# Optimization experiments

Hardware: AMD Instinct MI355X
Metric: run time of the kernel (lower is better)

The kernel has to match this reference:

```python
import jax, jax.numpy as jnp
import numpy as np

VOCAB, EMBED, HID, SEQ, BATCH = 32000, 256, 512, 128, 256
U1, U2 = 256, 64


def setup_inputs() -> dict:
    key = jax.random.key(0)
    ks = jax.random.split(key, 8)
    s = 0.05  # small init scale keeps relu-LSTM states bounded
    return {
        "inputs": jax.random.randint(ks[0], (BATCH, SEQ), 0, VOCAB),
        "emb": jax.random.normal(ks[1], (VOCAB, EMBED), jnp.float32) * s,
        "W": jax.random.normal(ks[2], (EMBED, 4 * HID), jnp.float32) * s,
        "U": jax.random.normal(ks[3], (HID, 4 * HID), jnp.float32) * s,
        "b": jnp.zeros((4 * HID,), jnp.float32),
        "W2": jax.random.normal(ks[4], (HID, U1), jnp.float32) * s,
        "b2": jnp.zeros((U1,), jnp.float32),
        "W3": jax.random.normal(ks[5], (U1, U2), jnp.float32) * s,
        "b3": jnp.zeros((U2,), jnp.float32),
    }


def reference(inputs, emb, W, U, b, W2, b2, W3, b3):
    H = U.shape[0]
    x = emb[inputs]                      # [B, T, E] embedding lookup
    xW = jnp.einsum('bte,eg->btg', x, W) + b  # precompute input gate projections [B, T, 4H]

    def step(carry, xw_t):
        h, c = carry
        z = xw_t + h @ U                 # [B, 4H]; Keras gate order i, f, c, o
        i = jax.nn.sigmoid(z[:, :H])
        f = jax.nn.sigmoid(z[:, H:2 * H])
        g = jax.nn.relu(z[:, 2 * H:3 * H])   # activation='relu'
        o = jax.nn.sigmoid(z[:, 3 * H:])
        c = f * c + i * g
        h = o * jax.nn.relu(c)
        return (h, c), None

    B = x.shape[0]
    init = (jnp.zeros((B, H), x.dtype), jnp.zeros((B, H), x.dtype))
    (h, _), _ = jax.lax.scan(step, init, jnp.swapaxes(xW, 0, 1))  # scan over time

    y = jax.nn.relu(h @ W2 + b2)         # Dense head 1
    return jax.nn.softmax(y @ W3 + b3, axis=-1)  # Dense head 2 (softmax)
```

## Files before the change

kernel.cpp:

```cpp
#include <hip/hip_runtime.h>
#include <hip/hip_bf16.h>
#include <stdint.h>

#define B_  256
#define T_  128
#define E_  256
#define H_  512
#define G4  2048
#define U1_ 256
#define U2_ 64

#define HB_STEP   (16 * 16 * 64 * 8)
#define XF_STEP   (16 * 8 * 64 * 8)
#define SGN 0x8000800080008000ULL

typedef __attribute__((ext_vector_type(8))) short bf16x8;
typedef __attribute__((ext_vector_type(4))) float f32x4;
typedef __attribute__((ext_vector_type(2))) unsigned long long ullx2;
typedef unsigned long long ull;

static __device__ __forceinline__ unsigned short f2bf(float f) {
    unsigned u = __float_as_uint(f);
    unsigned r = (u + 0x7FFFu + ((u >> 16) & 1u)) >> 16;
    return (unsigned short)r;
}
static __device__ __forceinline__ ull ald(const ull* p) {
    return __hip_atomic_load(p, __ATOMIC_RELAXED, __HIP_MEMORY_SCOPE_AGENT);
}
static __device__ __forceinline__ void ast(ull* p, ull v) {
    __hip_atomic_store(p, v, __ATOMIC_RELAXED, __HIP_MEMORY_SCOPE_AGENT);
}

__global__ __launch_bounds__(256) void k_prep(const float* __restrict__ U,
                                              const float* __restrict__ W,
                                              short* __restrict__ wpk) {
    __shared__ float ld[32][64];
    const int bj = blockIdx.x;
    const int g  = bj >> 3;
    const int l0 = (bj & 7) * 64;
    const int t  = threadIdx.x;
    const int p   = t >> 4;
    const int hsl = p >> 1, blk = p & 1;
    const int ci  = t & 3;
    const int g4w = (t >> 2) & 3;
    const int hs  = (l0 >> 3) + hsl;
    const int c16 = g * 4 + ci;
    const int jloc = hsl * 8 + blk * 4 + ci;
    for (int kc = 0; kc < 24; ++kc) {
        const float* src = (kc < 16) ? (U + (long)(kc * 32) * G4)
                                     : (W + (long)((kc - 16) * 32) * G4);
        #pragma unroll
        for (int r = 0; r < 8; ++r) {
            int row = r * 4 + (t >> 6);
            ld[row][t & 63] = src[(long)row * G4 + g * 512 + l0 + (t & 63)];
        }
        __syncthreads();
        bf16x8 o;
        #pragma unroll
        for (int e = 0; e < 8; ++e) o[e] = (short)f2bf(ld[g4w * 8 + e][jloc]);
        *(bf16x8*)(wpk + (((long)(hs * 2 + blk) * 24 + kc) * 64 + (g4w * 16 + c16)) * 8) = o;
        __syncthreads();
    }
}

__global__ __launch_bounds__(256) void k_gather(const int* __restrict__ inp,
                                                const float* __restrict__ emb,
                                                short* __restrict__ xfrag) {
    const int tid  = threadIdx.x;
    const int wv   = tid >> 6;
    const int lane = tid & 63;
    const int c16  = lane & 15;
    const int g4   = lane >> 4;
    for (int it = 0; it < 16; ++it) {
        int task  = (it * 256 + blockIdx.x) * 4 + wv;
        int kc    = task & 7;
        int btile = (task >> 3) & 15;
        int t     = task >> 7;
        int b     = btile * 16 + c16;
        int idx   = inp[b * T_ + t];
        const float* src = emb + (long)idx * E_ + kc * 32 + g4 * 8;
        float4 v0 = *(const float4*)src;
        float4 v1 = *(const float4*)(src + 4);
        bf16x8 o;
        o[0]=(short)f2bf(v0.x); o[1]=(short)f2bf(v0.y); o[2]=(short)f2bf(v0.z); o[3]=(short)f2bf(v0.w);
        o[4]=(short)f2bf(v1.x); o[5]=(short)f2bf(v1.y); o[6]=(short)f2bf(v1.z); o[7]=(short)f2bf(v1.w);
        *(bf16x8*)(xfrag + ((long)((t * 16 + btile) * 8 + kc) * 64 + lane) * 8) = o;
    }
}

__global__ __launch_bounds__(256, 1) void k_lstm(
    const float* __restrict__ bias,
    const short* __restrict__ wpk,
    const short* __restrict__ xfrag,
    short* hfrag,
    float* hfin)
{
    __shared__ short lds[2][16][64][8];
    const int tid  = threadIdx.x;
    const int wid  = blockIdx.x;
    const int bt   = wid >> 4;
    const int hsg  = wid & 15;
    const int lane = tid & 63;
    const int wv   = tid >> 6;
    const int hs   = hsg * 4 + wv;
    const int c16  = lane & 15;
    const int g4   = lane >> 4;
    const int selfj = ((hsg >> 2) == wv) ? (hsg & 3) : -1;

    bf16x8 a_u[2][16], a_w[2][8];
    #pragma unroll
    for (int blk = 0; blk < 2; ++blk) {
        #pragma unroll
        for (int kc = 0; kc < 16; ++kc)
            a_u[blk][kc] = *(const bf16x8*)(wpk + (((long)(hs*2+blk)*24 + kc)*64 + lane)*8);
        #pragma unroll
        for (int kc = 0; kc < 8; ++kc)
            a_w[blk][kc] = *(const bf16x8*)(wpk + (((long)(hs*2+blk)*24 + 16 + kc)*64 + lane)*8);
    }
    float b0[4], b1[4];
    #pragma unroll
    for (int q = 0; q < 4; ++q) {
        b0[q] = bias[g4 * H_ + hs * 8 + q];
        b1[q] = bias[g4 * H_ + hs * 8 + 4 + q];
    }
    float cst[8];
    #pragma unroll
    for (int i = 0; i < 8; ++i) cst[i] = 0.f;

    ull* const pub0 = (ull*)hfrag + (((long)bt * 16 + hsg) * 64 + wv * 16 + c16) * 2;

    for (int t = 0; t < T_; ++t) {
        const int cb = t & 1;
        ull L[4] = {0,0,0,0}, Hh[4] = {0,0,0,0};
        const ull* hp = (const ull*)hfrag + ((long)(t - 1) * HB_STEP) / 4;
        if (t > 0) {
            #pragma unroll
            for (int j = 0; j < 4; ++j) {
                const ull* p = hp + (((long)bt * 16 + (wv * 4 + j)) * 64 + lane) * 2;
                L[j]  = ald(p);
                Hh[j] = ald(p + 1);
            }
        }

        const short* xr = xfrag + (long)t * XF_STEP;
        bf16x8 xf[8];
        #pragma unroll
        for (int kc = 0; kc < 8; ++kc)
            xf[kc] = *(const bf16x8*)(xr + ((long)(bt * 8 + kc) * 64 + lane) * 8);

        f32x4 a0 = (f32x4){b0[0], b0[1], b0[2], b0[3]};
        f32x4 a1 = (f32x4){b1[0], b1[1], b1[2], b1[3]};
        #pragma unroll
        for (int kc = 0; kc < 8; ++kc) {
            a0 = __builtin_amdgcn_mfma_f32_16x16x32_bf16(a_w[0][kc], xf[kc], a0, 0, 0, 0);
            a1 = __builtin_amdgcn_mfma_f32_16x16x32_bf16(a_w[1][kc], xf[kc], a1, 0, 0, 0);
        }

        if (t > 0) {
            unsigned stale = 0xFu & ~((selfj >= 0) ? (1u << selfj) : 0u);
            for (int guard = 0; guard < (1 << 20); ++guard) {
                unsigned ns = 0;
                #pragma unroll
                for (int j = 0; j < 4; ++j) {
                    if ((stale >> j) & 1u) {
                        if (!__all(((L[j] | Hh[j]) & SGN) == 0)) ns |= (1u << j);
                    }
                }
                stale = ns;
                if (!stale) break;
                #pragma unroll
                for (int j = 0; j < 4; ++j) {
                    if ((stale >> j) & 1u) {
                        const ull* p = hp + (((long)bt * 16 + (wv * 4 + j)) * 64 + lane) * 2;
                        L[j]  = ald(p);
                        Hh[j] = ald(p + 1);
                    }
                }
            }
            #pragma unroll
            for (int j = 0; j < 4; ++j) {
                if (j != selfj) {
                    ullx2 u; u[0] = L[j]; u[1] = Hh[j];
                    *(ullx2*)(&lds[cb][wv * 4 + j][lane][0]) = u;
                }
            }
        }
        __syncthreads();

        if (t > 0) {
            #pragma unroll
            for (int kc = 0; kc < 16; ++kc) {
                bf16x8 hf = *(const bf16x8*)(&lds[cb][kc][lane][0]);
                a0 = __builtin_amdgcn_mfma_f32_16x16x32_bf16(a_u[0][kc], hf, a0, 0, 0, 0);
                a1 = __builtin_amdgcn_mfma_f32_16x16x32_bf16(a_u[1][kc], hf, a1, 0, 0, 0);
            }
        }

        float hv[8];
        #pragma unroll
        for (int blk = 0; blk < 2; ++blk) {
            #pragma unroll
            for (int q = 0; q < 4; ++q) {
                float z = blk ? a1[q] : a0[q];
                float a = (g4 == 2) ? fmaxf(z, 0.f)
                                    : 1.f / (1.f + __expf(-z));
                float ai = __shfl(a, c16,      64);
                float af = __shfl(a, c16 + 16, 64);
                float ag = __shfl(a, c16 + 32, 64);
                float ao = __shfl(a, c16 + 48, 64);
                float c_ = af * cst[blk*4+q] + ai * ag;
                cst[blk*4+q] = c_;
                hv[blk*4+q] = ao * fmaxf(c_, 0.f);
            }
        }

        if (t < T_ - 1) {
            if (g4 == 0) {
                ull p0 = (ull)f2bf(hv[0]) | ((ull)f2bf(hv[1])<<16)
                       | ((ull)f2bf(hv[2])<<32) | ((ull)f2bf(hv[3])<<48);
                ull p1 = (ull)f2bf(hv[4]) | ((ull)f2bf(hv[5])<<16)
                       | ((ull)f2bf(hv[6])<<32) | ((ull)f2bf(hv[7])<<48);
                ull* d = pub0 + (long)t * (HB_STEP / 4);
                ast(d, p0); ast(d + 1, p1);
                ullx2 u; u[0] = p0; u[1] = p1;
                *(ullx2*)(&lds[(t + 1) & 1][hsg][wv * 16 + c16][0]) = u;
            }
        } else {
            if (g4 == 0) {
                *(float4*)(hfin + ((long)bt * 16 + c16) * H_ + hs * 8)
                    = make_float4(hv[0], hv[1], hv[2], hv[3]);
                *(float4*)(hfin + ((long)bt * 16 + c16) * H_ + hs * 8 + 4)
                    = make_float4(hv[4], hv[5], hv[6], hv[7]);
            }
        }
    }
}

__global__ __launch_bounds__(256) void k_head(const float* __restrict__ hfin,
                                              const float* __restrict__ W2,
                                              const float* __restrict__ b2,
                                              const float* __restrict__ W3,
                                              const float* __restrict__ b3,
                                              float* __restrict__ out) {
    __shared__ float hs[H_];
    __shared__ float ys[U1_];
    __shared__ float ps[4][U2_];
    const int b = blockIdx.x, tid = threadIdx.x;
    if (tid < 128) *(float4*)(hs + tid * 4) = *(const float4*)(hfin + (long)b * H_ + tid * 4);
    __syncthreads();
    float acc = b2[tid];
    #pragma unroll 8
    for (int k = 0; k < H_; ++k) acc += hs[k] * W2[(long)k * U1_ + tid];
    ys[tid] = fmaxf(acc, 0.f);
    __syncthreads();
    const int u2 = tid & 63, part = tid >> 6;
    float p = 0.f;
    #pragma unroll 8
    for (int k = part * 64; k < part * 64 + 64; ++k) p += ys[k] * W3[(long)k * U2_ + u2];
    ps[part][u2] = p;
    __syncthreads();
    if (tid < 64) {
        float lg = b3[tid] + ps[0][tid] + ps[1][tid] + ps[2][tid] + ps[3][tid];
        float m = lg;
        #pragma unroll
        for (int off = 32; off >= 1; off >>= 1) m = fmaxf(m, __shfl_xor(m, off, 64));
        float e = __expf(lg - m);
        float s = e;
        #pragma unroll
        for (int off = 32; off >= 1; off >>= 1) s += __shfl_xor(s, off, 64);
        out[(long)b * U2_ + tid] = e / s;
    }
}

extern "C" void kernel_launch(void* const* d_in, const int* in_sizes, int n_in,
                              void* d_out, int out_size, void* d_ws, size_t ws_size,
                              hipStream_t stream) {
    const int*   inp = (const int*)d_in[0];
    const float* emb = (const float*)d_in[1];
    const float* W   = (const float*)d_in[2];
    const float* U   = (const float*)d_in[3];
    const float* bb  = (const float*)d_in[4];
    const float* W2  = (const float*)d_in[5];
    const float* b2  = (const float*)d_in[6];
    const float* W3  = (const float*)d_in[7];
    const float* b3  = (const float*)d_in[8];

    char* ws = (char*)d_ws;
    const long HB_BYTES = (long)(T_ - 1) * HB_STEP * 2;
    short* hfrag = (short*)ws;
    short* xfrag = (short*)(ws + HB_BYTES);
    short* wpk   = (short*)(ws + HB_BYTES + 16777216);
    float* hfin  = (float*)(ws + HB_BYTES + 16777216 + 3145728);

    hipMemsetAsync(hfrag, 0xAA, HB_BYTES, stream);
    k_prep<<<32, 256, 0, stream>>>(U, W, wpk);
    k_gather<<<256, 256, 0, stream>>>(inp, emb, xfrag);
    k_lstm<<<256, 256, 0, stream>>>(bb, wpk, xfrag, hfrag, hfin);
    k_head<<<B_, 256, 0, stream>>>(hfin, W2, b2, W3, b3, (float*)d_out);
}
```

Measured before the change: 528.6 us.

## Use 512-thread LSTM blocks covering 64 hidden units each, halving grid size

The persistent LSTM kernel now runs 128 blocks of 8 waves instead of 256 blocks of 4 waves. Each block owns two K-chunks of the hidden state, so each wave polls only two remote h fragments per step, and the wave whose chunks are local skips polling. The goal is less cross-block flag polling and global traffic per step, since more of the recurrent state is exchanged through LDS. In exchange, fewer CUs are used and the 8-wave __syncthreads barrier is wider, and each wave still keeps its full register-resident weight slices.

```diff
diff --git a/kernel.cpp b/kernel.cpp
--- a/kernel.cpp
+++ b/kernel.cpp
@@ -88,7 +88,7 @@
     }
 }
 
-__global__ __launch_bounds__(256, 1) void k_lstm(
+__global__ __launch_bounds__(512, 1) void k_lstm(
     const float* __restrict__ bias,
     const short* __restrict__ wpk,
     const short* __restrict__ xfrag,
@@ -98,14 +98,15 @@
     __shared__ short lds[2][16][64][8];
     const int tid  = threadIdx.x;
     const int wid  = blockIdx.x;
-    const int bt   = wid >> 4;
-    const int hsg  = wid & 15;
+    const int bt   = wid >> 3;
+    const int hh   = wid & 7;
     const int lane = tid & 63;
     const int wv   = tid >> 6;
-    const int hs   = hsg * 4 + wv;
+    const int hs   = hh * 8 + wv;
     const int c16  = lane & 15;
     const int g4   = lane >> 4;
-    const int selfj = ((hsg >> 2) == wv) ? (hsg & 3) : -1;
+    const int kcw  = hh * 2 + (wv >> 2);
+    const bool pollme = (wv != hh);
 
     bf16x8 a_u[2][16], a_w[2][8];
     #pragma unroll
@@ -127,16 +128,17 @@
     #pragma unroll
     for (int i = 0; i < 8; ++i) cst[i] = 0.f;
 
-    ull* const pub0 = (ull*)hfrag + (((long)bt * 16 + hsg) * 64 + wv * 16 + c16) * 2;
+    ull* const pub0 = (ull*)hfrag +
+        (((long)bt * 16 + kcw) * 64 + (wv & 3) * 16 + c16) * 2;
 
     for (int t = 0; t < T_; ++t) {
         const int cb = t & 1;
-        ull L[4] = {0,0,0,0}, Hh[4] = {0,0,0,0};
+        ull L[2], Hh[2];
         const ull* hp = (const ull*)hfrag + ((long)(t - 1) * HB_STEP) / 4;
-        if (t > 0) {
-            #pragma unroll
-            for (int j = 0; j < 4; ++j) {
-                const ull* p = hp + (((long)bt * 16 + (wv * 4 + j)) * 64 + lane) * 2;
+        if (t > 0 && pollme) {
+            #pragma unroll
+            for (int j = 0; j < 2; ++j) {
+                const ull* p = hp + (((long)bt * 16 + (wv * 2 + j)) * 64 + lane) * 2;
                 L[j]  = ald(p);
                 Hh[j] = ald(p + 1);
             }
@@ -156,33 +158,28 @@
             a1 = __builtin_amdgcn_mfma_f32_16x16x32_bf16(a_w[1][kc], xf[kc], a1, 0, 0, 0);
         }
 
-        if (t > 0) {
-            unsigned stale = 0xFu & ~((selfj >= 0) ? (1u << selfj) : 0u);
-            for (int guard = 0; guard < (1 << 20); ++guard) {
+        if (t > 0 && pollme) {
+            unsigned stale = 0x3u;
+            for (int g = 0; g < (1 << 20); ++g) {
                 unsigned ns = 0;
                 #pragma unroll
-                for (int j = 0; j < 4; ++j) {
-                    if ((stale >> j) & 1u) {
+                for (int j = 0; j < 2; ++j)
+                    if ((stale >> j) & 1u)
                         if (!__all(((L[j] | Hh[j]) & SGN) == 0)) ns |= (1u << j);
-                    }
-                }
                 stale = ns;
                 if (!stale) break;
                 #pragma unroll
-                for (int j = 0; j < 4; ++j) {
+                for (int j = 0; j < 2; ++j)
                     if ((stale >> j) & 1u) {
-                        const ull* p = hp + (((long)bt * 16 + (wv * 4 + j)) * 64 + lane) * 2;
+                        const ull* p = hp + (((long)bt * 16 + (wv * 2 + j)) * 64 + lane) * 2;
                         L[j]  = ald(p);
                         Hh[j] = ald(p + 1);
                     }
-                }
-            }
-            #pragma unroll
-            for (int j = 0; j < 4; ++j) {
-                if (j != selfj) {
-                    ullx2 u; u[0] = L[j]; u[1] = Hh[j];
-                    *(ullx2*)(&lds[cb][wv * 4 + j][lane][0]) = u;
-                }
+            }
+            #pragma unroll
+            for (int j = 0; j < 2; ++j) {
+                ullx2 u; u[0] = L[j]; u[1] = Hh[j];
+                *(ullx2*)(&lds[cb][wv * 2 + j][lane][0]) = u;
             }
         }
         __syncthreads();
@@ -223,7 +220,7 @@
                 ull* d = pub0 + (long)t * (HB_STEP / 4);
                 ast(d, p0); ast(d + 1, p1);
                 ullx2 u; u[0] = p0; u[1] = p1;
-                *(ullx2*)(&lds[(t + 1) & 1][hsg][wv * 16 + c16][0]) = u;
+                *(ullx2*)(&lds[(t + 1) & 1][kcw][(wv & 3) * 16 + c16][0]) = u;
             }
         } else {
             if (g4 == 0) {
@@ -295,6 +292,6 @@
     hipMemsetAsync(hfrag, 0xAA, HB_BYTES, stream);
     k_prep<<<32, 256, 0, stream>>>(U, W, wpk);
     k_gather<<<256, 256, 0, stream>>>(inp, emb, xfrag);
-    k_lstm<<<256, 256, 0, stream>>>(bb, wpk, xfrag, hfrag, hfin);
+    k_lstm<<<128, 512, 0, stream>>>(bb, wpk, xfrag, hfrag, hfin);
     k_head<<<B_, 256, 0, stream>>>(hfin, W2, b2, W3, b3, (float*)d_out);
 }
```

After: 665.0 us. 25.8% more time.

## Overlap cross-block h polling with MFMA and publish h halves early

Applied to the files above, without the earlier changes.

Reorders the recurrent step so the input-projection fragments are loaded before the remote h fragments. The spin-wait now double-buffers its polling loads (LA/LB) so one load is in flight while the other is checked. Fragments this wave fetched itself are fed straight from registers into the recurrent MFMAs before the barrier, and only the rest are read back from LDS. The first half of the new h is stored as soon as it is computed, so consumer blocks can see it sooner. The cost is more register pressure and more complex control flow in the sync loop.

```diff
diff --git a/kernel.cpp b/kernel.cpp
--- a/kernel.cpp
+++ b/kernel.cpp
@@ -131,22 +131,22 @@
 
     for (int t = 0; t < T_; ++t) {
         const int cb = t & 1;
-        ull L[4] = {0,0,0,0}, Hh[4] = {0,0,0,0};
         const ull* hp = (const ull*)hfrag + ((long)(t - 1) * HB_STEP) / 4;
+
+        const short* xr = xfrag + (long)t * XF_STEP;
+        bf16x8 xf[8];
+        #pragma unroll
+        for (int kc = 0; kc < 8; ++kc)
+            xf[kc] = *(const bf16x8*)(xr + ((long)(bt * 8 + kc) * 64 + lane) * 8);
+
+        ull LA[4], HA[4], LB[4], HB[4], L[4], Hh[4];
         if (t > 0) {
             #pragma unroll
-            for (int j = 0; j < 4; ++j) {
+            for (int j = 0; j < 4; ++j) if (j != selfj) {
                 const ull* p = hp + (((long)bt * 16 + (wv * 4 + j)) * 64 + lane) * 2;
-                L[j]  = ald(p);
-                Hh[j] = ald(p + 1);
-            }
-        }
-
-        const short* xr = xfrag + (long)t * XF_STEP;
-        bf16x8 xf[8];
-        #pragma unroll
-        for (int kc = 0; kc < 8; ++kc)
-            xf[kc] = *(const bf16x8*)(xr + ((long)(bt * 8 + kc) * 64 + lane) * 8);
+                LA[j] = ald(p); HA[j] = ald(p + 1);
+            }
+        }
 
         f32x4 a0 = (f32x4){b0[0], b0[1], b0[2], b0[3]};
         f32x4 a1 = (f32x4){b1[0], b1[1], b1[2], b1[3]};
@@ -158,31 +158,62 @@
 
         if (t > 0) {
             unsigned stale = 0xFu & ~((selfj >= 0) ? (1u << selfj) : 0u);
-            for (int guard = 0; guard < (1 << 20); ++guard) {
+            {
                 unsigned ns = 0;
                 #pragma unroll
-                for (int j = 0; j < 4; ++j) {
-                    if ((stale >> j) & 1u) {
-                        if (!__all(((L[j] | Hh[j]) & SGN) == 0)) ns |= (1u << j);
-                    }
+                for (int j = 0; j < 4; ++j) if ((stale >> j) & 1u) {
+                    if (__all(((LA[j] | HA[j]) & SGN) == 0)) { L[j] = LA[j]; Hh[j] = HA[j]; }
+                    else ns |= (1u << j);
                 }
                 stale = ns;
-                if (!stale) break;
+            }
+            if (stale) {
                 #pragma unroll
-                for (int j = 0; j < 4; ++j) {
-                    if ((stale >> j) & 1u) {
+                for (int j = 0; j < 4; ++j) if ((stale >> j) & 1u) {
+                    const ull* p = hp + (((long)bt * 16 + (wv * 4 + j)) * 64 + lane) * 2;
+                    LB[j] = ald(p); HB[j] = ald(p + 1);
+                }
+                for (int g = 0; g < (1 << 18); ++g) {
+                    #pragma unroll
+                    for (int j = 0; j < 4; ++j) if ((stale >> j) & 1u) {
                         const ull* p = hp + (((long)bt * 16 + (wv * 4 + j)) * 64 + lane) * 2;
-                        L[j]  = ald(p);
-                        Hh[j] = ald(p + 1);
+                        LA[j] = ald(p); HA[j] = ald(p + 1);
                     }
+                    unsigned ns = 0;
+                    #pragma unroll
+                    for (int j = 0; j < 4; ++j) if ((stale >> j) & 1u) {
+                        if (__all(((LB[j] | HB[j]) & SGN) == 0)) { L[j] = LB[j]; Hh[j] = HB[j]; }
+                        else ns |= (1u << j);
+                    }
+                    stale = ns;
+                    if (!stale) break;
+                    #pragma unroll
+                    for (int j = 0; j < 4; ++j) if ((stale >> j) & 1u) {
+                        const ull* p = hp + (((long)bt * 16 + (wv * 4 + j)) * 64 + lane) * 2;
+                        LB[j] = ald(p); HB[j] = ald(p + 1);
+                    }
+                    ns = 0;
+                    #pragma unroll
+                    for (int j = 0; j < 4; ++j) if ((stale >> j) & 1u) {
+                        if (__all(((LA[j] | HA[j]) & SGN) == 0)) { L[j] = LA[j]; Hh[j] = HA[j]; }
+                        else ns |= (1u << j);
+                    }
+                    stale = ns;
+                    if (!stale) break;
                 }
             }
             #pragma unroll
-            for (int j = 0; j < 4; ++j) {
-                if (j != selfj) {
-                    ullx2 u; u[0] = L[j]; u[1] = Hh[j];
-                    *(ullx2*)(&lds[cb][wv * 4 + j][lane][0]) = u;
-                }
+            for (int j = 0; j < 4; ++j) if (j != selfj) {
+                ullx2 u; u[0] = L[j]; u[1] = Hh[j];
+                *(ullx2*)(&lds[cb][wv * 4 + j][lane][0]) = u;
+            }
+            #pragma unroll
+            for (int kc = 0; kc < 16; ++kc) {
+                if ((kc >> 2) != wv || (kc & 3) == selfj) continue;
+                ullx2 u; u[0] = L[kc & 3]; u[1] = Hh[kc & 3];
+                bf16x8 hf = __builtin_bit_cast(bf16x8, u);
+                a0 = __builtin_amdgcn_mfma_f32_16x16x32_bf16(a_u[0][kc], hf, a0, 0, 0, 0);
+                a1 = __builtin_amdgcn_mfma_f32_16x16x32_bf16(a_u[1][kc], hf, a1, 0, 0, 0);
             }
         }
         __syncthreads();
@@ -190,38 +221,48 @@
         if (t > 0) {
             #pragma unroll
             for (int kc = 0; kc < 16; ++kc) {
+                if ((kc >> 2) == wv && (kc & 3) != selfj) continue;
                 bf16x8 hf = *(const bf16x8*)(&lds[cb][kc][lane][0]);
                 a0 = __builtin_amdgcn_mfma_f32_16x16x32_bf16(a_u[0][kc], hf, a0, 0, 0, 0);
                 a1 = __builtin_amdgcn_mfma_f32_16x16x32_bf16(a_u[1][kc], hf, a1, 0, 0, 0);
             }
         }
 
+        ull* const d = pub0 + (long)t * (HB_STEP / 4);
         float hv[8];
         #pragma unroll
-        for (int blk = 0; blk < 2; ++blk) {
-            #pragma unroll
-            for (int q = 0; q < 4; ++q) {
-                float z = blk ? a1[q] : a0[q];
-                float a = (g4 == 2) ? fmaxf(z, 0.f)
-                                    : 1.f / (1.f + __expf(-z));
-                float ai = __shfl(a, c16,      64);
-                float af = __shfl(a, c16 + 16, 64);
-                float ag = __shfl(a, c16 + 32, 64);
-                float ao = __shfl(a, c16 + 48, 64);
-                float c_ = af * cst[blk*4+q] + ai * ag;
-                cst[blk*4+q] = c_;
-                hv[blk*4+q] = ao * fmaxf(c_, 0.f);
-            }
-        }
+        for (int q = 0; q < 4; ++q) {
+            float z = a0[q];
+            float a = (g4 == 2) ? fmaxf(z, 0.f) : 1.f / (1.f + __expf(-z));
+            float ai = __shfl(a, c16,      64);
+            float af = __shfl(a, c16 + 16, 64);
+            float ag = __shfl(a, c16 + 32, 64);
+            float ao = __shfl(a, c16 + 48, 64);
+            float c_ = af * cst[q] + ai * ag;
+            cst[q] = c_;
+            hv[q] = ao * fmaxf(c_, 0.f);
+        }
+        ull p0 = (ull)f2bf(hv[0]) | ((ull)f2bf(hv[1])<<16)
+               | ((ull)f2bf(hv[2])<<32) | ((ull)f2bf(hv[3])<<48);
+        if (t < T_ - 1 && g4 == 0) ast(d, p0);
+        #pragma unroll
+        for (int q = 0; q < 4; ++q) {
+            float z = a1[q];
+            float a = (g4 == 2) ? fmaxf(z, 0.f) : 1.f / (1.f + __expf(-z));
+            float ai = __shfl(a, c16,      64);
+            float af = __shfl(a, c16 + 16, 64);
+            float ag = __shfl(a, c16 + 32, 64);
+            float ao = __shfl(a, c16 + 48, 64);
+            float c_ = af * cst[4 + q] + ai * ag;
+            cst[4 + q] = c_;
+            hv[4 + q] = ao * fmaxf(c_, 0.f);
+        }
+        ull p1 = (ull)f2bf(hv[4]) | ((ull)f2bf(hv[5])<<16)
+               | ((ull)f2bf(hv[6])<<32) | ((ull)f2bf(hv[7])<<48);
 
         if (t < T_ - 1) {
             if (g4 == 0) {
-                ull p0 = (ull)f2bf(hv[0]) | ((ull)f2bf(hv[1])<<16)
-                       | ((ull)f2bf(hv[2])<<32) | ((ull)f2bf(hv[3])<<48);
-                ull p1 = (ull)f2bf(hv[4]) | ((ull)f2bf(hv[5])<<16)
-                       | ((ull)f2bf(hv[6])<<32) | ((ull)f2bf(hv[7])<<48);
-                ull* d = pub0 + (long)t * (HB_STEP / 4);
-                ast(d, p0); ast(d + 1, p1);
+                ast(d + 1, p1);
                 ullx2 u; u[0] = p0; u[1] = p1;
                 *(ullx2*)(&lds[(t + 1) & 1][hsg][wv * 16 + c16][0]) = u;
             }
```

New measurement: 507.6 us. 4.0% less time.
